# Optimization experiments

Measured on AMD Instinct MI355X. Metric: run time of the kernel, lower is better.

Reference implementation:

```python
import jax, jax.numpy as jnp
import numpy as np

N_NODES = 50000
NEG_SLOPE = 0.2  # PyG GATv2Conv default negative_slope


def _gatv2_layer(x, src, dst, W_l, W_r, att, bias, num_nodes):
    """Single-head GATv2Conv (PyG semantics, flow source_to_target)."""
    x_l = x @ W_l  # [N, C] source-side transform
    x_r = x @ W_r  # [N, C] target-side transform
    h = x_l[src] + x_r[dst]                      # [E, C] per-edge pre-activation
    h = jnp.where(h > 0, h, NEG_SLOPE * h)       # LeakyReLU
    e = h @ att                                  # [E] unnormalized attention logits
    # segment softmax over destination nodes (stable)
    e_max = jax.ops.segment_max(e, dst, num_segments=num_nodes)
    e_exp = jnp.exp(e - e_max[dst])
    denom = jax.ops.segment_sum(e_exp, dst, num_segments=num_nodes)
    alpha = e_exp / denom[dst]                   # [E]
    out = jax.ops.segment_sum(x_l[src] * alpha[:, None], dst, num_segments=num_nodes)
    return out + bias, alpha


def setup_inputs() -> dict:
    key = jax.random.key(0)
    ks = jax.random.split(key, 12)
    N, E, T, D = N_NODES, 800000, 512, 128
    g = lambda k, shp, fan_in: jax.random.normal(k, shp, dtype=jnp.float32) / np.sqrt(fan_in)
    return {
        "x": jax.random.normal(ks[0], (N, T), dtype=jnp.float32),
        "edge_index": jax.random.randint(ks[1], (2, E), 0, N, dtype=jnp.int64 if jax.config.jax_enable_x64 else jnp.int32),
        "mmse_score": jax.random.uniform(ks[2], (1,), dtype=jnp.float32),
        "W_l1": g(ks[3], (T, D), T),
        "W_r1": g(ks[4], (T, D), T),
        "att1": g(ks[5], (D,), D),
        "bias1": jnp.zeros((D,), jnp.float32),
        "W_l2": g(ks[6], (D, D), D),
        "W_r2": g(ks[7], (D, D), D),
        "att2": g(ks[8], (D,), D),
        "bias2": jnp.zeros((D,), jnp.float32),
        "mmse_W": g(ks[9], (1, D), 1),
        "mmse_b": jnp.zeros((D,), jnp.float32),
    }


def reference(x, edge_index, mmse_score, W_l1, W_r1, att1, bias1,
              W_l2, W_r2, att2, bias2, mmse_W, mmse_b):
    N = x.shape[0]
    # PyG add_self_loops=True: append one self-loop per node
    loops = jnp.arange(N, dtype=edge_index.dtype)
    src = jnp.concatenate([edge_index[0], loops])
    dst = jnp.concatenate([edge_index[1], loops])

    attn_features1, attn_weights = _gatv2_layer(x, src, dst, W_l1, W_r1, att1, bias1, N)
    # attn_weights is detached in the original (torch.tensor(...)); layer 2 ignores
    # the passed edge_attr (edge_dim=None -> no lin_edge) and recomputes attention.
    attn_weights = jax.lax.stop_gradient(attn_weights)
    graph_features, _ = _gatv2_layer(attn_features1, src, dst, W_l2, W_r2, att2, bias2, N)
    mmse_embedded = mmse_score @ mmse_W + mmse_b  # [D]
    graph_features = graph_features + mmse_embedded
    return graph_features, attn_weights
```

## Files before the change

kernel.cpp:

```cpp
#include <hip/hip_runtime.h>
#include <cstdint>

typedef __bf16 bf16;
typedef __bf16 bf16x8 __attribute__((ext_vector_type(8)));
typedef float f32x4 __attribute__((ext_vector_type(4)));

__device__ __forceinline__ void load_lds16(const void* g, void* l) {
  __builtin_amdgcn_global_load_lds(
      (const __attribute__((address_space(1))) void*)g,
      (__attribute__((address_space(3))) void*)l, 16, 0, 0);
}

__device__ __forceinline__ unsigned short bf16_bits(float f) {
  return __builtin_bit_cast(unsigned short, (bf16)f);
}
__device__ __forceinline__ float bf_lo(unsigned u) {
  return __uint_as_float(u << 16);
}
__device__ __forceinline__ float bf_hi(unsigned u) {
  return __uint_as_float(u & 0xffff0000u);
}

__global__ void hist_kernel(const int* __restrict__ ei, int E, int N,
                            int* __restrict__ counts) {
  const int total = E + N;
  for (int i = blockIdx.x * blockDim.x + threadIdx.x; i < total;
       i += gridDim.x * blockDim.x) {
    const int d = (i < E) ? ei[E + i] : (i - E);
    atomicAdd(&counts[d], 1);
  }
}

__global__ void scan_reduce(const int* __restrict__ counts,
                            int* __restrict__ bsum, int N) {
  __shared__ int red[256];
  const int chunk = (N + 255) / 256;
  const int lo = blockIdx.x * chunk;
  const int hi = min(lo + chunk, N);
  int s = 0;
  for (int i = lo + threadIdx.x; i < hi; i += 256) s += counts[i];
  red[threadIdx.x] = s;
  __syncthreads();
  for (int off = 128; off; off >>= 1) {
    if (threadIdx.x < off) red[threadIdx.x] += red[threadIdx.x + off];
    __syncthreads();
  }
  if (threadIdx.x == 0) bsum[blockIdx.x] = red[0];
}

__global__ void scan_bsum(int* __restrict__ bsum, int* __restrict__ row_ptr,
                          int N) {
  __shared__ int tmp[256];
  const int tid = threadIdx.x;
  const int v = bsum[tid];
  tmp[tid] = v;
  __syncthreads();
  for (int off = 1; off < 256; off <<= 1) {
    const int t = (tid >= off) ? tmp[tid - off] : 0;
    __syncthreads();
    tmp[tid] += t;
    __syncthreads();
  }
  bsum[tid] = tmp[tid] - v;
  if (tid == 255) row_ptr[N] = tmp[255];
}

__global__ void scan_write(const int* __restrict__ counts,
                           const int* __restrict__ boff,
                           int* __restrict__ row_ptr, int* __restrict__ cursor,
                           int N) {
  __shared__ int tmp[256];
  const int chunk = (N + 255) / 256;
  const int lo = blockIdx.x * chunk;
  const int hi = min(lo + chunk, N);
  int carry = boff[blockIdx.x];
  for (int base = lo; base < hi; base += 256) {
    const int i = base + threadIdx.x;
    const int v = (i < hi) ? counts[i] : 0;
    tmp[threadIdx.x] = v;
    __syncthreads();
    for (int off = 1; off < 256; off <<= 1) {
      const int t = (threadIdx.x >= off) ? tmp[threadIdx.x - off] : 0;
      __syncthreads();
      tmp[threadIdx.x] += t;
      __syncthreads();
    }
    if (i < hi) {
      const int excl = carry + tmp[threadIdx.x] - v;
      row_ptr[i] = excl;
      cursor[i] = excl;
    }
    carry += tmp[255];
    __syncthreads();
  }
}

__global__ void scatter_kernel(const int* __restrict__ ei, int E, int N,
                               int* __restrict__ cursor,
                               int* __restrict__ csr_src,
                               int* __restrict__ csr_eid) {
  const int total = E + N;
  for (int i = blockIdx.x * blockDim.x + threadIdx.x; i < total;
       i += gridDim.x * blockDim.x) {
    int s, d;
    if (i < E) { s = ei[i]; d = ei[E + i]; } else { s = d = i - E; }
    const int pos = atomicAdd(&cursor[d], 1);
    csr_src[pos] = s;
    csr_eid[pos] = i;
  }
}

__global__ void mmse_kernel(const float* __restrict__ score,
                            const float* __restrict__ W,
                            const float* __restrict__ b,
                            float* __restrict__ out, int D) {
  const int i = threadIdx.x;
  if (i < D) out[i] = score[0] * W[i] + b[i];
}

__global__ void wt_kernel(const float* __restrict__ Wl,
                          const float* __restrict__ Wr,
                          bf16* __restrict__ Wt, int K) {
  const int idx = blockIdx.x * blockDim.x + threadIdx.x;
  if (idx >= 256 * K) return;
  const int col = idx & 255;
  const int k = idx >> 8;
  const float v = (col < 128) ? Wl[k * 128 + col] : Wr[k * 128 + (col - 128)];
  Wt[(size_t)col * K + k] = (bf16)v;
}

template <bool AF32>
__global__ __launch_bounds__(512) void gemm_mfma(
    const void* __restrict__ Ap, const bf16* __restrict__ Wt,
    bf16* __restrict__ xl, bf16* __restrict__ xr, int M, int K) {
  __shared__ __align__(16) bf16 Alds[128 * 32];
  __shared__ __align__(16) bf16 Blds[256 * 32];

  const int tid = threadIdx.x;
  const int w = tid >> 6, lane = tid & 63;
  const int wr = w >> 2, wc = w & 3;
  const int row0 = blockIdx.x * 128;

  const int s_row = tid >> 2;
  const int s_k = (tid & 3) * 8;
  const int a_row = min(row0 + s_row, M - 1);
  bf16* a_dst = Alds + tid * 8;

  const int b_col0 = w * 32 + (lane >> 2);
  const bf16* b_src0 = Wt + (size_t)b_col0 * K + (lane & 3) * 8;
  const bf16* b_src1 = Wt + (size_t)(b_col0 + 16) * K + (lane & 3) * 8;
  bf16* b_dst0 = Blds + w * 1024 + lane * 8;
  bf16* b_dst1 = b_dst0 + 512;

  const int a_f0 = (wr * 64 + (lane & 15)) * 32 + (lane >> 4) * 8;
  const int b_f0 = (wc * 64 + (lane & 15)) * 32 + (lane >> 4) * 8;

  f32x4 acc[4][4] = {};

  for (int k0 = 0; k0 < K; k0 += 32) {
    bf16x8 av;
    if (AF32) {
      const float* A = (const float*)Ap;
      const float4 f0 = *(const float4*)&A[(size_t)a_row * K + k0 + s_k];
      const float4 f1 = *(const float4*)&A[(size_t)a_row * K + k0 + s_k + 4];
      av[0] = (bf16)f0.x; av[1] = (bf16)f0.y; av[2] = (bf16)f0.z; av[3] = (bf16)f0.w;
      av[4] = (bf16)f1.x; av[5] = (bf16)f1.y; av[6] = (bf16)f1.z; av[7] = (bf16)f1.w;
    } else {
      av = *(const bf16x8*)((const bf16*)Ap + (size_t)a_row * K + k0 + s_k);
    }
    __syncthreads();
    *(bf16x8*)a_dst = av;
    load_lds16(b_src0 + k0, b_dst0);
    load_lds16(b_src1 + k0, b_dst1);
    __syncthreads();

    bf16x8 af[4], bfr[4];
#pragma unroll
    for (int m = 0; m < 4; ++m) af[m] = *(const bf16x8*)(Alds + a_f0 + m * 512);
#pragma unroll
    for (int n = 0; n < 4; ++n) bfr[n] = *(const bf16x8*)(Blds + b_f0 + n * 512);
#pragma unroll
    for (int m = 0; m < 4; ++m)
#pragma unroll
      for (int n = 0; n < 4; ++n)
        acc[m][n] = __builtin_amdgcn_mfma_f32_16x16x32_bf16(af[m], bfr[n],
                                                            acc[m][n], 0, 0, 0);
  }

#pragma unroll
  for (int m = 0; m < 4; ++m) {
    const int rbase = row0 + wr * 64 + m * 16 + (lane >> 4) * 4;
#pragma unroll
    for (int n = 0; n < 4; ++n) {
      const int c = wc * 64 + n * 16 + (lane & 15);
      bf16* dst = (c < 128) ? xl : xr;
      const int cc = c & 127;
#pragma unroll
      for (int j = 0; j < 4; ++j) {
        const int r = rbase + j;
        if (r < M) dst[(size_t)r * 128 + cc] = (bf16)acc[m][n][j];
      }
    }
  }
}

__global__ __launch_bounds__(256) void gat_edge(
    const bf16* __restrict__ xl, const bf16* __restrict__ xr,
    const int* __restrict__ row_ptr, const int* __restrict__ csr_src,
    const int* __restrict__ csr_eid, const float* __restrict__ att,
    const float* __restrict__ bias, const float* __restrict__ extra,
    bf16* __restrict__ out_b,
    float* __restrict__ out_f,
    float* __restrict__ e_ws, float* __restrict__ m_ws,
    float* __restrict__ den_ws, int N) {
  const int wave = threadIdx.x >> 6;
  const int lane = threadIdx.x & 63;
  const int l5 = lane & 31;
  const int half = lane >> 5;
  const int node_raw = blockIdx.x * 8 + wave * 2 + half;
  const bool vnode = node_raw < N;
  const int node = vnode ? node_raw : N - 1;

  const int d0 = l5 * 4;
  const float4 attv = *(const float4*)&att[d0];
  const uint2 ur = *(const uint2*)&xr[(size_t)node * 128 + d0];
  const float r0 = bf_lo(ur.x), r1 = bf_hi(ur.x);
  const float r2 = bf_lo(ur.y), r3 = bf_hi(ur.y);

  float m = -1e30f, den = 0.f;
  float a0 = 0.f, a1 = 0.f, a2 = 0.f, a3 = 0.f;

  const int beg = vnode ? row_ptr[node] : 0;
  const int end = vnode ? row_ptr[node + 1] : 0;
  const int nbat = (end - beg + 7) >> 3;
  const int nloop = max(nbat, __shfl_xor(nbat, 32));

  for (int t = 0; t < nloop; ++t) {
    const int idx = beg + t * 8;

    int s[8];
#pragma unroll
    for (int j = 0; j < 8; ++j) {
      const int k = idx + j;
      s[j] = csr_src[(k < end) ? k : beg];
    }
    int eid[8];
    if (e_ws != nullptr) {
#pragma unroll
      for (int j = 0; j < 8; ++j) {
        const int k = idx + j;
        eid[j] = csr_eid[(k < end) ? k : beg];
      }
    }

    uint2 u[8];
#pragma unroll
    for (int j = 0; j < 8; ++j)
      u[j] = *(const uint2*)&xl[(size_t)s[j] * 128 + d0];

    float p[8];
#pragma unroll
    for (int j = 0; j < 8; ++j) {
      float h0 = bf_lo(u[j].x) + r0;
      float h1 = bf_hi(u[j].x) + r1;
      float h2 = bf_lo(u[j].y) + r2;
      float h3 = bf_hi(u[j].y) + r3;
      h0 = h0 > 0.f ? h0 : 0.2f * h0;
      h1 = h1 > 0.f ? h1 : 0.2f * h1;
      h2 = h2 > 0.f ? h2 : 0.2f * h2;
      h3 = h3 > 0.f ? h3 : 0.2f * h3;
      p[j] = fmaf(h0, attv.x, fmaf(h1, attv.y, fmaf(h2, attv.z, h3 * attv.w)));
    }

#pragma unroll
    for (int off = 16; off; off >>= 1) {
#pragma unroll
      for (int j = 0; j < 8; ++j) p[j] += __shfl_xor(p[j], off);
    }

#pragma unroll
    for (int j = 0; j < 8; ++j)
      if (idx + j >= end) p[j] = -1e30f;

    if (e_ws != nullptr && l5 == 0) {
#pragma unroll
      for (int j = 0; j < 8; ++j)
        if (idx + j < end) e_ws[eid[j]] = p[j];
    }

    const float bm = fmaxf(fmaxf(fmaxf(p[0], p[1]), fmaxf(p[2], p[3])),
                           fmaxf(fmaxf(p[4], p[5]), fmaxf(p[6], p[7])));
    if (bm > m) {
      const float f = __expf(m - bm);
      den *= f;
      a0 *= f; a1 *= f; a2 *= f; a3 *= f;
      m = bm;
    }
#pragma unroll
    for (int j = 0; j < 8; ++j) {
      const float wgt = __expf(p[j] - m);
      den += wgt;
      a0 = fmaf(wgt, bf_lo(u[j].x), a0);
      a1 = fmaf(wgt, bf_hi(u[j].x), a1);
      a2 = fmaf(wgt, bf_lo(u[j].y), a2);
      a3 = fmaf(wgt, bf_hi(u[j].y), a3);
    }
  }

  if (!vnode) return;

  const float inv = 1.f / den;
  const float4 bv = *(const float4*)&bias[d0];
  float o0 = fmaf(a0, inv, bv.x);
  float o1 = fmaf(a1, inv, bv.y);
  float o2 = fmaf(a2, inv, bv.z);
  float o3 = fmaf(a3, inv, bv.w);
  if (extra != nullptr) {
    const float4 ev = *(const float4*)&extra[d0];
    o0 += ev.x; o1 += ev.y; o2 += ev.z; o3 += ev.w;
  }
  if (out_b != nullptr) {
    uint2 pk;
    pk.x = (unsigned)bf16_bits(o0) | ((unsigned)bf16_bits(o1) << 16);
    pk.y = (unsigned)bf16_bits(o2) | ((unsigned)bf16_bits(o3) << 16);
    *(uint2*)&out_b[(size_t)node * 128 + d0] = pk;
  }
  if (out_f != nullptr) {
    float4 ov; ov.x = o0; ov.y = o1; ov.z = o2; ov.w = o3;
    *(float4*)&out_f[(size_t)node * 128 + d0] = ov;
  }
  if (m_ws != nullptr && l5 == 0) {
    m_ws[node] = m;
    den_ws[node] = den;
  }
}

__global__ void alpha_kernel(const float* __restrict__ e_ws,
                             const float* __restrict__ m_ws,
                             const float* __restrict__ den_ws,
                             const int* __restrict__ ei, int E, int N,
                             float* __restrict__ out_alpha) {
  const int i = blockIdx.x * blockDim.x + threadIdx.x;
  if (i >= E + N) return;
  const int d = (i < E) ? ei[E + i] : (i - E);
  out_alpha[i] = __expf(e_ws[i] - m_ws[d]) / den_ws[d];
}

extern "C" void kernel_launch(void* const* d_in, const int* in_sizes, int n_in,
                              void* d_out, int out_size, void* d_ws,
                              size_t ws_size, hipStream_t stream) {
  const float* x          = (const float*)d_in[0];
  const int*   ei         = (const int*)d_in[1];
  const float* mmse_score = (const float*)d_in[2];
  const float* W_l1       = (const float*)d_in[3];
  const float* W_r1       = (const float*)d_in[4];
  const float* att1       = (const float*)d_in[5];
  const float* bias1      = (const float*)d_in[6];
  const float* W_l2       = (const float*)d_in[7];
  const float* W_r2       = (const float*)d_in[8];
  const float* att2       = (const float*)d_in[9];
  const float* bias2      = (const float*)d_in[10];
  const float* mmse_W     = (const float*)d_in[11];
  const float* mmse_b     = (const float*)d_in[12];

  const int D  = in_sizes[5];
  const int T  = in_sizes[3] / D;
  const int N  = in_sizes[0] / T;
  const int E  = in_sizes[1] / 2;
  const int ET = E + N;

  char* wptr = (char*)d_ws;
  auto alloc = [&](size_t bytes) {
    char* p = wptr;
    wptr += (bytes + 255) & ~(size_t)255;
    return p;
  };
  bf16* xl      = (bf16*)alloc((size_t)N * 128 * 2);
  bf16* xr      = (bf16*)alloc((size_t)N * 128 * 2);
  bf16* attn1   = (bf16*)alloc((size_t)N * 128 * 2);
  bf16* Wt1     = (bf16*)alloc((size_t)256 * T * 2);
  bf16* Wt2     = (bf16*)alloc((size_t)256 * D * 2);
  float* e_ws   = (float*)alloc((size_t)ET * 4);
  float* m_ws   = (float*)alloc((size_t)N * 4);
  float* den_ws = (float*)alloc((size_t)N * 4);
  float* mmse_vec = (float*)alloc(512);
  int* counts  = (int*)alloc((size_t)N * 4);
  int* row_ptr = (int*)alloc((size_t)(N + 1) * 4);
  int* cursor  = (int*)alloc((size_t)N * 4);
  int* bsum    = (int*)alloc(256 * 4);
  int* csr_src = (int*)alloc((size_t)ET * 4);
  int* csr_eid = (int*)alloc((size_t)ET * 4);

  float* out_feat  = (float*)d_out;
  float* out_alpha = out_feat + (size_t)N * D;

  hipMemsetAsync(counts, 0, (size_t)N * 4, stream);
  hist_kernel<<<2048, 256, 0, stream>>>(ei, E, N, counts);
  scan_reduce<<<256, 256, 0, stream>>>(counts, bsum, N);
  scan_bsum<<<1, 256, 0, stream>>>(bsum, row_ptr, N);
  scan_write<<<256, 256, 0, stream>>>(counts, bsum, row_ptr, cursor, N);
  scatter_kernel<<<2048, 256, 0, stream>>>(ei, E, N, cursor, csr_src, csr_eid);

  wt_kernel<<<(256 * T + 255) / 256, 256, 0, stream>>>(W_l1, W_r1, Wt1, T);
  wt_kernel<<<(256 * D + 255) / 256, 256, 0, stream>>>(W_l2, W_r2, Wt2, D);
  mmse_kernel<<<1, 128, 0, stream>>>(mmse_score, mmse_W, mmse_b, mmse_vec, D);

  const int gblocks = (N + 127) / 128;
  gemm_mfma<true><<<gblocks, 512, 0, stream>>>(x, Wt1, xl, xr, N, T);

  gat_edge<<<(N + 7) / 8, 256, 0, stream>>>(xl, xr, row_ptr, csr_src, csr_eid,
                                            att1, bias1, nullptr, attn1,
                                            nullptr, e_ws, m_ws, den_ws, N);

  alpha_kernel<<<(ET + 255) / 256, 256, 0, stream>>>(e_ws, m_ws, den_ws, ei, E,
                                                     N, out_alpha);

  gemm_mfma<false><<<gblocks, 512, 0, stream>>>(attn1, Wt2, xl, xr, N, D);

  gat_edge<<<(N + 7) / 8, 256, 0, stream>>>(xl, xr, row_ptr, csr_src, csr_eid,
                                            att2, bias2, mmse_vec, nullptr,
                                            out_feat, nullptr, nullptr, nullptr,
                                            N);
}
```

Baseline: 447.3 us.

## Prefetch next edge batch in gat_edge and store logits in CSR order

The edge loop now double-buffers: it loads the next batch of 8 source indices and xl rows while computing on the current batch, so gather latency can overlap with compute. Separately, the csr_eid array is replaced by a pos_of inverse map written in scatter. Layer-1 logits are stored at their CSR position (coalesced), and alpha_kernel gathers through pos_of, which removes the eid loads from gat_edge. The cost is more registers from the doubled buffers, which may lower occupancy, plus a random gather in alpha_kernel.

```diff
diff --git a/kernel.cpp b/kernel.cpp
--- a/kernel.cpp
+++ b/kernel.cpp
@@ -98,7 +98,7 @@
 __global__ void scatter_kernel(const int* __restrict__ ei, int E, int N,
                                int* __restrict__ cursor,
                                int* __restrict__ csr_src,
-                               int* __restrict__ csr_eid) {
+                               int* __restrict__ pos_of) {
   const int total = E + N;
   for (int i = blockIdx.x * blockDim.x + threadIdx.x; i < total;
        i += gridDim.x * blockDim.x) {
@@ -106,7 +106,7 @@
     if (i < E) { s = ei[i]; d = ei[E + i]; } else { s = d = i - E; }
     const int pos = atomicAdd(&cursor[d], 1);
     csr_src[pos] = s;
-    csr_eid[pos] = i;
+    pos_of[i] = pos;
   }
 }
 
@@ -207,8 +207,8 @@
 __global__ __launch_bounds__(256) void gat_edge(
     const bf16* __restrict__ xl, const bf16* __restrict__ xr,
     const int* __restrict__ row_ptr, const int* __restrict__ csr_src,
-    const int* __restrict__ csr_eid, const float* __restrict__ att,
-    const float* __restrict__ bias, const float* __restrict__ extra,
+    const float* __restrict__ att, const float* __restrict__ bias,
+    const float* __restrict__ extra,
     bf16* __restrict__ out_b,
     float* __restrict__ out_f,
     float* __restrict__ e_ws, float* __restrict__ m_ws,
@@ -235,36 +235,40 @@
   const int nbat = (end - beg + 7) >> 3;
   const int nloop = max(nbat, __shfl_xor(nbat, 32));
 
+  int sA[8];
+#pragma unroll
+  for (int j = 0; j < 8; ++j) {
+    const int k = beg + j;
+    sA[j] = csr_src[(k < end) ? k : beg];
+  }
+  uint2 uA[8];
+#pragma unroll
+  for (int j = 0; j < 8; ++j)
+    uA[j] = *(const uint2*)&xl[(size_t)sA[j] * 128 + d0];
+
   for (int t = 0; t < nloop; ++t) {
     const int idx = beg + t * 8;
-
-    int s[8];
+    const bool more = (t + 1 < nloop);
+    const int nxt = idx + 8;
+
+    int sB[8];
 #pragma unroll
     for (int j = 0; j < 8; ++j) {
-      const int k = idx + j;
-      s[j] = csr_src[(k < end) ? k : beg];
-    }
-    int eid[8];
-    if (e_ws != nullptr) {
-#pragma unroll
-      for (int j = 0; j < 8; ++j) {
-        const int k = idx + j;
-        eid[j] = csr_eid[(k < end) ? k : beg];
-      }
-    }
-
-    uint2 u[8];
+      const int k = nxt + j;
+      sB[j] = csr_src[(more && k < end) ? k : beg];
+    }
+    uint2 uB[8];
 #pragma unroll
     for (int j = 0; j < 8; ++j)
-      u[j] = *(const uint2*)&xl[(size_t)s[j] * 128 + d0];
+      uB[j] = *(const uint2*)&xl[(size_t)sB[j] * 128 + d0];
 
     float p[8];
 #pragma unroll
     for (int j = 0; j < 8; ++j) {
-      float h0 = bf_lo(u[j].x) + r0;
-      float h1 = bf_hi(u[j].x) + r1;
-      float h2 = bf_lo(u[j].y) + r2;
-      float h3 = bf_hi(u[j].y) + r3;
+      float h0 = bf_lo(uA[j].x) + r0;
+      float h1 = bf_hi(uA[j].x) + r1;
+      float h2 = bf_lo(uA[j].y) + r2;
+      float h3 = bf_hi(uA[j].y) + r3;
       h0 = h0 > 0.f ? h0 : 0.2f * h0;
       h1 = h1 > 0.f ? h1 : 0.2f * h1;
       h2 = h2 > 0.f ? h2 : 0.2f * h2;
@@ -285,7 +289,7 @@
     if (e_ws != nullptr && l5 == 0) {
 #pragma unroll
       for (int j = 0; j < 8; ++j)
-        if (idx + j < end) e_ws[eid[j]] = p[j];
+        if (idx + j < end) e_ws[idx + j] = p[j];
     }
 
     const float bm = fmaxf(fmaxf(fmaxf(p[0], p[1]), fmaxf(p[2], p[3])),
@@ -300,10 +304,16 @@
     for (int j = 0; j < 8; ++j) {
       const float wgt = __expf(p[j] - m);
       den += wgt;
-      a0 = fmaf(wgt, bf_lo(u[j].x), a0);
-      a1 = fmaf(wgt, bf_hi(u[j].x), a1);
-      a2 = fmaf(wgt, bf_lo(u[j].y), a2);
-      a3 = fmaf(wgt, bf_hi(u[j].y), a3);
+      a0 = fmaf(wgt, bf_lo(uA[j].x), a0);
+      a1 = fmaf(wgt, bf_hi(uA[j].x), a1);
+      a2 = fmaf(wgt, bf_lo(uA[j].y), a2);
+      a3 = fmaf(wgt, bf_hi(uA[j].y), a3);
+    }
+
+#pragma unroll
+    for (int j = 0; j < 8; ++j) {
+      sA[j] = sB[j];
+      uA[j] = uB[j];
     }
   }
 
@@ -338,12 +348,14 @@
 __global__ void alpha_kernel(const float* __restrict__ e_ws,
                              const float* __restrict__ m_ws,
                              const float* __restrict__ den_ws,
-                             const int* __restrict__ ei, int E, int N,
+                             const int* __restrict__ ei,
+                             const int* __restrict__ pos_of, int E, int N,
                              float* __restrict__ out_alpha) {
   const int i = blockIdx.x * blockDim.x + threadIdx.x;
   if (i >= E + N) return;
   const int d = (i < E) ? ei[E + i] : (i - E);
-  out_alpha[i] = __expf(e_ws[i] - m_ws[d]) / den_ws[d];
+  const int pos = pos_of[i];
+  out_alpha[i] = __expf(e_ws[pos] - m_ws[d]) / den_ws[d];
 }
 
 extern "C" void kernel_launch(void* const* d_in, const int* in_sizes, int n_in,
@@ -389,7 +401,7 @@
   int* cursor  = (int*)alloc((size_t)N * 4);
   int* bsum    = (int*)alloc(256 * 4);
   int* csr_src = (int*)alloc((size_t)ET * 4);
-  int* csr_eid = (int*)alloc((size_t)ET * 4);
+  int* pos_of  = (int*)alloc((size_t)ET * 4);
 
   float* out_feat  = (float*)d_out;
   float* out_alpha = out_feat + (size_t)N * D;
@@ -399,7 +411,7 @@
   scan_reduce<<<256, 256, 0, stream>>>(counts, bsum, N);
   scan_bsum<<<1, 256, 0, stream>>>(bsum, row_ptr, N);
   scan_write<<<256, 256, 0, stream>>>(counts, bsum, row_ptr, cursor, N);
-  scatter_kernel<<<2048, 256, 0, stream>>>(ei, E, N, cursor, csr_src, csr_eid);
+  scatter_kernel<<<2048, 256, 0, stream>>>(ei, E, N, cursor, csr_src, pos_of);
 
   wt_kernel<<<(256 * T + 255) / 256, 256, 0, stream>>>(W_l1, W_r1, Wt1, T);
   wt_kernel<<<(256 * D + 255) / 256, 256, 0, stream>>>(W_l2, W_r2, Wt2, D);
@@ -408,17 +420,16 @@
   const int gblocks = (N + 127) / 128;
   gemm_mfma<true><<<gblocks, 512, 0, stream>>>(x, Wt1, xl, xr, N, T);
 
-  gat_edge<<<(N + 7) / 8, 256, 0, stream>>>(xl, xr, row_ptr, csr_src, csr_eid,
-                                            att1, bias1, nullptr, attn1,
-                                            nullptr, e_ws, m_ws, den_ws, N);
-
-  alpha_kernel<<<(ET + 255) / 256, 256, 0, stream>>>(e_ws, m_ws, den_ws, ei, E,
-                                                     N, out_alpha);
+  gat_edge<<<(N + 7) / 8, 256, 0, stream>>>(xl, xr, row_ptr, csr_src, att1,
+                                            bias1, nullptr, attn1, nullptr,
+                                            e_ws, m_ws, den_ws, N);
+
+  alpha_kernel<<<(ET + 255) / 256, 256, 0, stream>>>(e_ws, m_ws, den_ws, ei,
+                                                     pos_of, E, N, out_alpha);
 
   gemm_mfma<false><<<gblocks, 512, 0, stream>>>(attn1, Wt2, xl, xr, N, D);
 
-  gat_edge<<<(N + 7) / 8, 256, 0, stream>>>(xl, xr, row_ptr, csr_src, csr_eid,
-                                            att2, bias2, mmse_vec, nullptr,
-                                            out_feat, nullptr, nullptr, nullptr,
-                                            N);
-}
+  gat_edge<<<(N + 7) / 8, 256, 0, stream>>>(xl, xr, row_ptr, csr_src, att2,
+                                            bias2, mmse_vec, nullptr, out_feat,
+                                            nullptr, nullptr, nullptr, N);
+}
```

After: 517.6 us. 15.7% more time.
